# Kernel tuning notes

Hardware: AMD Instinct MI355X
Metric: run time of the kernel (lower is better)

## Reference

```python
import jax, jax.numpy as jnp
import numpy as np

RES = 0.1
TABLE = 1 << 20  # hash_table_size, power of two
PRIMES = np.array([73856093, 19349669, 83492791], dtype=np.int64)
FEAT_DIM = 120
BMIN = (-2.6, -8.1, 0.0)
BMAX = (4.6, 4.7, 3.1)
M_QUERIES = 1_000_000
CORNERS = np.array([[0,0,0],[1,0,0],[0,1,0],[0,0,1],[1,1,0],[1,0,1],[0,1,1],[1,1,1]], dtype=np.int32)


def _build_table():
    # Replicates build_hash_grid(): first-come voxel index per hash slot, collisions skipped.
    xs = np.arange(BMIN[0], BMAX[0], RES, dtype=np.float32)
    ys = np.arange(BMIN[1], BMAX[1], RES, dtype=np.float32)
    zs = np.arange(BMIN[2], BMAX[2], RES, dtype=np.float32)
    gx, gy, gz = np.meshgrid(xs, ys, zs, indexing='ij')
    coords = np.stack([gx, gy, gz], -1).reshape(-1, 3)
    gc = np.floor(coords / RES).astype(np.int64)
    h = np.remainder((gc * PRIMES).sum(-1), TABLE)
    n = coords.shape[0]
    buf = np.full(TABLE, -1, dtype=np.int32)
    buf[h[::-1]] = np.arange(n, dtype=np.int32)[::-1]
    return buf, n


def setup_inputs() -> dict:
    key = jax.random.key(0)
    k1, k2 = jax.random.split(key)
    buf, n_vox = _build_table()
    lo = jnp.array(BMIN, jnp.float32)
    hi = jnp.array(BMAX, jnp.float32)
    query_pts = lo + (hi - lo) * jax.random.uniform(k1, (M_QUERIES, 3), dtype=jnp.float32)
    features = 0.01 * jax.random.normal(k2, (n_vox, FEAT_DIM), dtype=jnp.float32)
    return {
        "query_pts": query_pts,
        "features": features,
        "buffer_voxel_index": jnp.asarray(buf),  # int32 [TABLE]
    }


def reference(query_pts, features, buffer_voxel_index):
    """query_voxel_feature with trilinear_feat=True: 8-corner hash lookup + trilinear blend."""
    primes_u = jnp.asarray(PRIMES.astype(np.uint32))
    gcf = query_pts / RES                        # [M,3]
    floor = jnp.floor(gcf)
    frac = gcf - floor                           # [M,3]
    base = floor.astype(jnp.int32)               # [M,3]
    acc = jnp.zeros((query_pts.shape[0], features.shape[1]), dtype=features.dtype)
    for c in CORNERS:                            # fixed 8-iteration corner loop
        cj = jnp.asarray(c)
        cc = base + cj                           # [M,3]
        # TABLE is a power of two, so low-20-bits of wrapping uint32 arithmetic
        # equals the exact int64 remainder used by torch.
        h = ((cc.astype(jnp.uint32) * primes_u).sum(-1) & (TABLE - 1)).astype(jnp.int32)
        vidx = buffer_voxel_index[h]             # [M], -1 for empty slots
        w = jnp.where(cj == 0, 1.0 - frac, frac).prod(-1)  # [M] trilinear weight
        w = jnp.where(vidx >= 0, w, 0.0)
        acc = acc + features[jnp.maximum(vidx, 0)] * w[:, None]
    return acc
```

## Files before the change

kernel.cpp:

```cpp
#include <hip/hip_runtime.h>


#define TABLE_MASK ((1u << 20) - 1u)
#define FEAT_DIM 120
#define ROW_STRIDE 120
#define NROWS 27
#define NCHUNK 30
#define NXCD 8
#define C8 12

#define NBINS_X 64
#define NBINS_Y 128
#define NBINS_Z 16
#define NBINS (NBINS_X * NBINS_Y * NBINS_Z)

typedef float f4 __attribute__((ext_vector_type(4)));

__global__ __launch_bounds__(256) void zero_kernel(int* __restrict__ hist8) {
    const int i = blockIdx.x * blockDim.x + threadIdx.x;
    if (i < NXCD * NBINS + 2) hist8[i] = 0;
}

__global__ __launch_bounds__(256) void bin_kernel(
    const float* __restrict__ qp, int* __restrict__ hist8,
    f4* __restrict__ sq8, f4* __restrict__ ovf, int Cr, int M)
{
    const int q = blockIdx.x * blockDim.x + threadIdx.x;
    if (q >= M) return;

    int xcd;
    asm volatile("s_getreg_b32 %0, hwreg(HW_REG_XCC_ID)" : "=s"(xcd));
    xcd &= (NXCD - 1);

    const float gx = qp[3 * q + 0] / 0.1f;
    const float gy = qp[3 * q + 1] / 0.1f;
    const float gz = qp[3 * q + 2] / 0.1f;
    const int bx = (int)floorf(gx);
    const int by = (int)floorf(gy);
    const int bz = (int)floorf(gz);
    const int kx = ((bx + 32) >> 1) & (NBINS_X - 1);
    const int ky = ((by + 96) >> 1) & (NBINS_Y - 1);
    const int kz = (bz >> 1) & (NBINS_Z - 1);
    const int key = ((kx * NBINS_Y) + ky) * NBINS_Z + kz;

    const int pos = __hip_atomic_fetch_add(&hist8[xcd * NBINS + key], 1,
                                           __ATOMIC_RELAXED,
                                           __HIP_MEMORY_SCOPE_WORKGROUP);
    f4 s;
    s.x = gx; s.y = gy; s.z = gz; s.w = __int_as_float(q);
    if (pos < Cr) {
        sq8[((size_t)xcd * NBINS + key) * C8 + pos] = s;
    } else {
        const int o = atomicAdd(&hist8[NXCD * NBINS], 1);
        if (o < M) ovf[o] = s;
    }
}

__global__ __launch_bounds__(256) void compact_kernel(
    const int* __restrict__ hist8, int* __restrict__ nact,
    int* __restrict__ list)
{
    const int i = blockIdx.x * blockDim.x + threadIdx.x;
    if (i >= NBINS) return;
    int tot = 0;
#pragma unroll
    for (int s = 0; s < NXCD; ++s) tot += hist8[s * NBINS + i];
    if (tot > 0) {
        const int p = atomicAdd(nact, 1);
        list[p] = i;
    }
}

__global__ __launch_bounds__(256, 8) void voxel_trilinear_kernel(
    const f4*    __restrict__ sq8,
    const float* __restrict__ feat,
    const int*   __restrict__ table,
    const int*   __restrict__ hist8,
    const int*   __restrict__ nactp,
    const int*   __restrict__ list,
    float*       __restrict__ out,
    int Cr)
{
    __shared__ int   cnt_s[NXCD];
    __shared__ int   pre_s[NXCD + 1];
    __shared__ int   vox[NROWS];
    __shared__ f4    sqL[NXCD * C8];
    __shared__ float rows[NROWS * ROW_STRIDE];

    const int t = threadIdx.x;
    const int nact = *nactp;

    for (int bi = blockIdx.x; bi < nact; bi += gridDim.x) {
        const int wg = list[bi];
        __syncthreads();

        if (t < NXCD) {
            int c = hist8[t * NBINS + wg];
            cnt_s[t] = (c > Cr) ? Cr : c;
        }
        __syncthreads();
        if (t == 0) {
            int acc = 0;
            pre_s[0] = 0;
#pragma unroll
            for (int i = 0; i < NXCD; ++i) { acc += cnt_s[i]; pre_s[i + 1] = acc; }
        }
        __syncthreads();
        const int total = pre_s[NXCD];

        const int binx = wg >> 11;
        const int biny = (wg >> 4) & 127;
        const int binz = wg & 15;
        const int vx0 = binx * 2 - 32;
        const int vy0 = biny * 2 - 96;
        const int vz0 = binz * 2;

        if (t < NROWS) {
            const int i = t / 9;
            const int j = (t / 3) % 3;
            const int k = t % 3;
            const unsigned h = (unsigned)(vx0 + i) * 73856093u
                             + (unsigned)(vy0 + j) * 19349669u
                             + (unsigned)(vz0 + k) * 83492791u;
            vox[t] = table[h & TABLE_MASK];
        }
        if (t >= 128) {
            const int seg = (t - 128) >> 4;
            const int lane16 = t & 15;
            if (lane16 < cnt_s[seg])
                sqL[pre_s[seg] + lane16] =
                    sq8[((size_t)seg * NBINS + wg) * C8 + lane16];
        }
        __syncthreads();

        for (int idx = t; idx < NROWS * NCHUNK; idx += 256) {
            const int row = idx / NCHUNK;
            const int chunk = idx - row * NCHUNK;
            const int v = vox[row];
            f4 val = (f4)(0.0f);
            if (v >= 0)
                val = *reinterpret_cast<const f4*>(
                    feat + (size_t)v * FEAT_DIM + chunk * 4);
            *reinterpret_cast<f4*>(rows + row * ROW_STRIDE + chunk * 4) = val;
        }
        __syncthreads();

        const int group = t >> 4;
        const int l = t & 15;
        const int CX[8] = {0, 1, 0, 0, 1, 1, 0, 1};
        const int CY[8] = {0, 0, 1, 0, 1, 0, 1, 1};
        const int CZ[8] = {0, 0, 0, 1, 0, 1, 1, 1};

        for (int qs = group; qs < total; qs += 16) {
            const f4 qv = sqL[qs];
            const float rx = qv.x - floorf(qv.x);
            const float ry = qv.y - floorf(qv.y);
            const float rz = qv.z - floorf(qv.z);
            const int q = __float_as_int(qv.w);
            const int lx = ((int)floorf(qv.x) + 32) & 1;
            const int ly = ((int)floorf(qv.y) + 96) & 1;
            const int lz = (int)floorf(qv.z) & 1;

            const float sx = 1.0f - rx, sy = 1.0f - ry, sz = 1.0f - rz;
            float w[8];
            w[0] = sx * sy * sz;
            w[1] = rx * sy * sz;
            w[2] = sx * ry * sz;
            w[3] = sx * sy * rz;
            w[4] = rx * ry * sz;
            w[5] = rx * sy * rz;
            w[6] = sx * ry * rz;
            w[7] = rx * ry * rz;

            f4 a0 = (f4)(0.0f), a1 = (f4)(0.0f);
#pragma unroll
            for (int k = 0; k < 8; ++k) {
                const int row = ((lx + CX[k]) * 3 + (ly + CY[k])) * 3 + (lz + CZ[k]);
                const float* rp = rows + row * ROW_STRIDE;
                const f4 fa = *reinterpret_cast<const f4*>(rp + l * 4);
                const f4 fb = *reinterpret_cast<const f4*>(rp + 56 + l * 4);
                a0 += fa * w[k];
                a1 += fb * w[k];
            }

            float* po = out + (size_t)q * FEAT_DIM;
            __builtin_nontemporal_store(a0, reinterpret_cast<f4*>(po + l * 4));
            if (l >= 2)
                __builtin_nontemporal_store(a1, reinterpret_cast<f4*>(po + 56 + l * 4));
        }
    }
}

__global__ __launch_bounds__(256) void ovf_kernel(
    const f4*    __restrict__ ovf,
    const int*   __restrict__ hist8,
    const float* __restrict__ feat,
    const int*   __restrict__ table,
    float*       __restrict__ out,
    int M)
{
    int n = hist8[NXCD * NBINS];
    if (n > M) n = M;
    if (n == 0) return;

    const int nthreads = gridDim.x * 256;
    for (int i = blockIdx.x * 256 + threadIdx.x; i < n * 16; i += nthreads) {
        const int g = i >> 4;
        const int l = i & 15;
        const f4 qv = ovf[g];
        const float gx = qv.x, gy = qv.y, gz = qv.z;
        const int q = __float_as_int(qv.w);
        const float flx = floorf(gx), fly = floorf(gy), flz = floorf(gz);
        const float rx = gx - flx, ry = gy - fly, rz = gz - flz;
        const int bx = (int)flx, by = (int)fly, bz = (int)flz;

        const unsigned hx0 = (unsigned)bx * 73856093u;
        const unsigned hy0 = (unsigned)by * 19349669u;
        const unsigned hz0 = (unsigned)bz * 83492791u;
        const unsigned hx1 = hx0 + 73856093u;
        const unsigned hy1 = hy0 + 19349669u;
        const unsigned hz1 = hz0 + 83492791u;

        unsigned h[8];
        h[0] = (hx0 + hy0 + hz0) & TABLE_MASK;
        h[1] = (hx1 + hy0 + hz0) & TABLE_MASK;
        h[2] = (hx0 + hy1 + hz0) & TABLE_MASK;
        h[3] = (hx0 + hy0 + hz1) & TABLE_MASK;
        h[4] = (hx1 + hy1 + hz0) & TABLE_MASK;
        h[5] = (hx1 + hy0 + hz1) & TABLE_MASK;
        h[6] = (hx0 + hy1 + hz1) & TABLE_MASK;
        h[7] = (hx1 + hy1 + hz1) & TABLE_MASK;

        int vidx[8];
#pragma unroll
        for (int k = 0; k < 8; ++k) vidx[k] = table[h[k]];

        const float sxw = 1.0f - rx, syw = 1.0f - ry, szw = 1.0f - rz;
        float w[8];
        w[0] = sxw * syw * szw;
        w[1] = rx  * syw * szw;
        w[2] = sxw * ry  * szw;
        w[3] = sxw * syw * rz;
        w[4] = rx  * ry  * szw;
        w[5] = rx  * syw * rz;
        w[6] = sxw * ry  * rz;
        w[7] = rx  * ry  * rz;

        f4 a0 = (f4)(0.0f), a1 = (f4)(0.0f);
#pragma unroll
        for (int k = 0; k < 8; ++k) {
            const int v = vidx[k] >= 0 ? vidx[k] : 0;
            const float wk = vidx[k] >= 0 ? w[k] : 0.0f;
            const float* rp = feat + (size_t)v * FEAT_DIM;
            const f4 fa = *reinterpret_cast<const f4*>(rp + l * 4);
            const f4 fb = *reinterpret_cast<const f4*>(rp + 56 + l * 4);
            a0 += fa * wk;
            a1 += fb * wk;
        }

        float* po = out + (size_t)q * FEAT_DIM;
        __builtin_nontemporal_store(a0, reinterpret_cast<f4*>(po + l * 4));
        if (l >= 2)
            __builtin_nontemporal_store(a1, reinterpret_cast<f4*>(po + 56 + l * 4));
    }
}

extern "C" void kernel_launch(void* const* d_in, const int* in_sizes, int n_in,
                              void* d_out, int out_size, void* d_ws, size_t ws_size,
                              hipStream_t stream) {
    const float* qp    = (const float*)d_in[0];
    const float* feat  = (const float*)d_in[1];
    const int*   table = (const int*)d_in[2];
    float*       out   = (float*)d_out;

    const int M = in_sizes[0] / 3;

    const size_t histB = ((NXCD * NBINS + 2) * sizeof(int) + 15) & ~(size_t)15;
    const size_t listB = (NBINS * sizeof(int) + 15) & ~(size_t)15;
    int* hist8 = (int*)d_ws;
    int* nact  = hist8 + NXCD * NBINS + 1;
    int* list  = (int*)((char*)d_ws + histB);
    f4*  ovf   = (f4*)((char*)d_ws + histB + listB);
    f4*  sq8   = ovf + M;

    const size_t fixed = histB + listB + (size_t)M * 16;
    size_t cap = (ws_size > fixed)
               ? (ws_size - fixed) / ((size_t)NXCD * NBINS * 16) : 0;
    int Cr = (cap > C8) ? C8 : (int)cap;
    if (Cr < 1) Cr = 1;

    const int block = 256;
    zero_kernel<<<(NXCD * NBINS + 2 + block - 1) / block, block, 0, stream>>>(hist8);
    bin_kernel<<<(M + block - 1) / block, block, 0, stream>>>(qp, hist8, sq8, ovf, Cr, M);
    compact_kernel<<<(NBINS + block - 1) / block, block, 0, stream>>>(hist8, nact, list);
    voxel_trilinear_kernel<<<2048, 256, 0, stream>>>(sq8, feat, table, hist8,
                                                     nact, list, out, Cr);
    ovf_kernel<<<512, 256, 0, stream>>>(ovf, hist8, feat, table, out, M);
}
```

Baseline: 261.4 us.

## Enlarge bins to 4x4x2 voxels and register-prefetch next bin's features

Bins now cover 4x4x2 voxels (a 5x5x3 halo of 75 feature rows) instead of 2x2x2 (27 rows), which cuts the redundant halo gathers per query. The per-bin setup is rewritten as a software pipeline: each thread loads the next bin's hash lookups, feature chunks and query records into registers while the current bin is computed, so the global gathers overlap the shared-memory blend. Blocks grow to 512 threads and per-bin query capacity to 32 per XCD. The cost is more registers and shared memory per block, lower occupancy, and fewer, larger bins that may balance load less evenly.

Result: faster. 234.5 us (-10.3%).

```diff
diff --git a/kernel.cpp b/kernel.cpp
--- a/kernel.cpp
+++ b/kernel.cpp
@@ -4,13 +4,15 @@
 #define TABLE_MASK ((1u << 20) - 1u)
 #define FEAT_DIM 120
 #define ROW_STRIDE 120
-#define NROWS 27
+#define NROWS 75
 #define NCHUNK 30
+#define TOTCH (NROWS * NCHUNK)
+#define NSLOT 5
 #define NXCD 8
-#define C8 12
-
-#define NBINS_X 64
-#define NBINS_Y 128
+#define C8 32
+
+#define NBINS_X 32
+#define NBINS_Y 64
 #define NBINS_Z 16
 #define NBINS (NBINS_X * NBINS_Y * NBINS_Z)
 
@@ -38,8 +40,8 @@
     const int bx = (int)floorf(gx);
     const int by = (int)floorf(gy);
     const int bz = (int)floorf(gz);
-    const int kx = ((bx + 32) >> 1) & (NBINS_X - 1);
-    const int ky = ((by + 96) >> 1) & (NBINS_Y - 1);
+    const int kx = ((bx + 32) >> 2) & (NBINS_X - 1);
+    const int ky = ((by + 96) >> 2) & (NBINS_Y - 1);
     const int kz = (bz >> 1) & (NBINS_Z - 1);
     const int key = ((kx * NBINS_Y) + ky) * NBINS_Z + kz;
 
@@ -71,7 +73,7 @@
     }
 }
 
-__global__ __launch_bounds__(256, 8) void voxel_trilinear_kernel(
+__global__ __launch_bounds__(512, 4) void voxel_trilinear_kernel(
     const f4*    __restrict__ sq8,
     const float* __restrict__ feat,
     const int*   __restrict__ table,
@@ -81,69 +83,90 @@
     float*       __restrict__ out,
     int Cr)
 {
-    __shared__ int   cnt_s[NXCD];
-    __shared__ int   pre_s[NXCD + 1];
-    __shared__ int   vox[NROWS];
     __shared__ f4    sqL[NXCD * C8];
     __shared__ float rows[NROWS * ROW_STRIDE];
 
     const int t = threadIdx.x;
     const int nact = *nactp;
-
-    for (int bi = blockIdx.x; bi < nact; bi += gridDim.x) {
-        const int wg = list[bi];
+    const int stride = gridDim.x;
+
+    if (blockIdx.x >= nact) return;
+
+    f4   rreg[NSLOT];
+    f4   qreg;
+    bool qok = false;
+    int  qdst = 0;
+    int  total = 0;
+
+    auto prefetch = [&](int wg) {
+        int c[8];
+#pragma unroll
+        for (int i = 0; i < 8; ++i) {
+            int v = hist8[i * NBINS + wg];
+            c[i] = (v > Cr) ? Cr : v;
+        }
+        total = 0;
+#pragma unroll
+        for (int i = 0; i < 8; ++i) total += c[i];
+
+        qok = false;
+        if (t < 256) {
+            const int seg = t >> 5, lane = t & 31;
+            int p = 0;
+#pragma unroll
+            for (int i = 0; i < 8; ++i) p += (i < seg) ? c[i] : 0;
+            if (lane < c[seg]) {
+                qok = true;
+                qdst = p + lane;
+                qreg = sq8[((size_t)seg * NBINS + wg) * C8 + lane];
+            }
+        }
+
+        const int binx = wg >> 10;
+        const int biny = (wg >> 4) & 63;
+        const int binz = wg & 15;
+        const int vx0 = binx * 4 - 32;
+        const int vy0 = biny * 4 - 96;
+        const int vz0 = binz * 2;
+#pragma unroll
+        for (int s = 0; s < NSLOT; ++s) {
+            const int idx = t + s * 512;
+            f4 val = (f4)(0.0f);
+            if (idx < TOTCH) {
+                const int row = idx / NCHUNK;
+                const int chunk = idx - row * NCHUNK;
+                const int i = row / 15;
+                const int j = (row / 3) % 5;
+                const int k = row % 3;
+                const unsigned h = (unsigned)(vx0 + i) * 73856093u
+                                 + (unsigned)(vy0 + j) * 19349669u
+                                 + (unsigned)(vz0 + k) * 83492791u;
+                const int v = table[h & TABLE_MASK];
+                if (v >= 0)
+                    val = *reinterpret_cast<const f4*>(
+                        feat + (size_t)v * FEAT_DIM + chunk * 4);
+            }
+            rreg[s] = val;
+        }
+    };
+
+    prefetch(list[blockIdx.x]);
+
+    for (int bi = blockIdx.x; bi < nact; bi += stride) {
         __syncthreads();
 
-        if (t < NXCD) {
-            int c = hist8[t * NBINS + wg];
-            cnt_s[t] = (c > Cr) ? Cr : c;
-        }
+#pragma unroll
+        for (int s = 0; s < NSLOT; ++s) {
+            const int idx = t + s * 512;
+            if (idx < TOTCH)
+                *reinterpret_cast<f4*>(rows + idx * 4) = rreg[s];
+        }
+        if (qok) sqL[qdst] = qreg;
+        const int ct = total;
         __syncthreads();
-        if (t == 0) {
-            int acc = 0;
-            pre_s[0] = 0;
-#pragma unroll
-            for (int i = 0; i < NXCD; ++i) { acc += cnt_s[i]; pre_s[i + 1] = acc; }
-        }
-        __syncthreads();
-        const int total = pre_s[NXCD];
-
-        const int binx = wg >> 11;
-        const int biny = (wg >> 4) & 127;
-        const int binz = wg & 15;
-        const int vx0 = binx * 2 - 32;
-        const int vy0 = biny * 2 - 96;
-        const int vz0 = binz * 2;
-
-        if (t < NROWS) {
-            const int i = t / 9;
-            const int j = (t / 3) % 3;
-            const int k = t % 3;
-            const unsigned h = (unsigned)(vx0 + i) * 73856093u
-                             + (unsigned)(vy0 + j) * 19349669u
-                             + (unsigned)(vz0 + k) * 83492791u;
-            vox[t] = table[h & TABLE_MASK];
-        }
-        if (t >= 128) {
-            const int seg = (t - 128) >> 4;
-            const int lane16 = t & 15;
-            if (lane16 < cnt_s[seg])
-                sqL[pre_s[seg] + lane16] =
-                    sq8[((size_t)seg * NBINS + wg) * C8 + lane16];
-        }
-        __syncthreads();
-
-        for (int idx = t; idx < NROWS * NCHUNK; idx += 256) {
-            const int row = idx / NCHUNK;
-            const int chunk = idx - row * NCHUNK;
-            const int v = vox[row];
-            f4 val = (f4)(0.0f);
-            if (v >= 0)
-                val = *reinterpret_cast<const f4*>(
-                    feat + (size_t)v * FEAT_DIM + chunk * 4);
-            *reinterpret_cast<f4*>(rows + row * ROW_STRIDE + chunk * 4) = val;
-        }
-        __syncthreads();
+
+        const int nb = bi + stride;
+        if (nb < nact) prefetch(list[nb]);
 
         const int group = t >> 4;
         const int l = t & 15;
@@ -151,14 +174,14 @@
         const int CY[8] = {0, 0, 1, 0, 1, 0, 1, 1};
         const int CZ[8] = {0, 0, 0, 1, 0, 1, 1, 1};
 
-        for (int qs = group; qs < total; qs += 16) {
+        for (int qs = group; qs < ct; qs += 32) {
             const f4 qv = sqL[qs];
             const float rx = qv.x - floorf(qv.x);
             const float ry = qv.y - floorf(qv.y);
             const float rz = qv.z - floorf(qv.z);
             const int q = __float_as_int(qv.w);
-            const int lx = ((int)floorf(qv.x) + 32) & 1;
-            const int ly = ((int)floorf(qv.y) + 96) & 1;
+            const int lx = ((int)floorf(qv.x) + 32) & 3;
+            const int ly = ((int)floorf(qv.y) + 96) & 3;
             const int lz = (int)floorf(qv.z) & 1;
 
             const float sx = 1.0f - rx, sy = 1.0f - ry, sz = 1.0f - rz;
@@ -175,7 +198,7 @@
             f4 a0 = (f4)(0.0f), a1 = (f4)(0.0f);
 #pragma unroll
             for (int k = 0; k < 8; ++k) {
-                const int row = ((lx + CX[k]) * 3 + (ly + CY[k])) * 3 + (lz + CZ[k]);
+                const int row = ((lx + CX[k]) * 5 + (ly + CY[k])) * 3 + (lz + CZ[k]);
                 const float* rp = rows + row * ROW_STRIDE;
                 const f4 fa = *reinterpret_cast<const f4*>(rp + l * 4);
                 const f4 fb = *reinterpret_cast<const f4*>(rp + 56 + l * 4);
@@ -293,7 +316,7 @@
     zero_kernel<<<(NXCD * NBINS + 2 + block - 1) / block, block, 0, stream>>>(hist8);
     bin_kernel<<<(M + block - 1) / block, block, 0, stream>>>(qp, hist8, sq8, ovf, Cr, M);
     compact_kernel<<<(NBINS + block - 1) / block, block, 0, stream>>>(hist8, nact, list);
-    voxel_trilinear_kernel<<<2048, 256, 0, stream>>>(sq8, feat, table, hist8,
+    voxel_trilinear_kernel<<<1024, 512, 0, stream>>>(sq8, feat, table, hist8,
                                                      nact, list, out, Cr);
     ovf_kernel<<<512, 256, 0, stream>>>(ovf, hist8, feat, table, out, M);
 }
```
